# Optimization experiments

Hardware: AMD Instinct MI355X
Metric: run time of the kernel (lower is better)

The kernel has to match this reference:

```python
import jax, jax.numpy as jnp
import numpy as np

N_ITERATIONS = 3  # matches init_kwargs n_iterations


def squash(s):
    # s: [batch, output_caps, output_dim]
    sq = jnp.sum(s * s, axis=2, keepdims=True)          # [b, oc, 1]
    return s * (sq / (1.0 + sq) / jnp.sqrt(sq))


def setup_inputs() -> dict:
    key = jax.random.key(0)
    k_u, = jax.random.split(key, 1)
    batch, ic, oc, od = 128, 2048, 32, 16
    u_predict = jax.random.normal(k_u, (batch, ic, oc, od), dtype=jnp.float32)
    b = jnp.zeros((ic, oc), dtype=jnp.float32)  # routing logit prior, init zeros per torch module
    return {"u_predict": u_predict, "b": b}


def reference(u_predict, b):
    # u_predict: [batch, input_caps, output_caps, output_dim]; b: [input_caps, output_caps]
    batch = u_predict.shape[0]
    c = jax.nn.softmax(b, axis=1)                              # softmax over output_caps (torch implicit dim=1 on 2D)
    s = jnp.einsum('io,biod->bod', c, u_predict)               # weighted sum over input_caps
    v = squash(s)
    b_batch = jnp.broadcast_to(b, (batch,) + b.shape)          # [b, ic, oc]
    for _ in range(N_ITERATIONS):
        b_batch = b_batch + jnp.einsum('biod,bod->bio', u_predict, v)  # agreement
        c = jax.nn.softmax(b_batch, axis=-1)                   # coupling coeffs over output_caps
        s = jnp.einsum('bio,biod->bod', c, u_predict)
        v = squash(s)
    return v
```

## Files before the change

kernel.cpp:

```cpp
#include <hip/hip_runtime.h>
#include <math.h>


namespace {
constexpr int BATCH = 128;
constexpr int IC    = 2048;
constexpr int OC    = 32;
constexpr int OD    = 16;
constexpr int ROW   = OC * OD;
constexpr int BPB   = 16;
constexpr int ROWS_PER_BLOCK = IC / BPB;
constexpr int NWAVES = 4;

typedef _Float16 half8 __attribute__((ext_vector_type(8)));
typedef float    f32x4 __attribute__((ext_vector_type(4)));

constexpr size_t OFF_U16  = 0;
constexpr size_t OFF_PART = 268435456;
constexpr size_t OFF_W    = OFF_PART + 4194304;
constexpr size_t OFF_C0   = OFF_W + 262144;
}

__global__ void __launch_bounds__(256)
softmax_b(const float* __restrict__ blogit, float* __restrict__ c0)
{
    const int idx = blockIdx.x * 256 + threadIdx.x;
    float x = blogit[idx];
    float m = x;
#pragma unroll
    for (int off = 1; off <= 16; off <<= 1)
        m = fmaxf(m, __shfl_xor(m, off, 64));
    float e = __expf(x - m);
    float s = e;
#pragma unroll
    for (int off = 1; off <= 16; off <<= 1)
        s += __shfl_xor(s, off, 64);
    c0[idx] = e / s;
}

__global__ void __launch_bounds__(256)
pass0_convert(const float* __restrict__ u, const float* __restrict__ c0,
              _Float16* __restrict__ u16, float* __restrict__ partials)
{
    const int tid = threadIdx.x, lane = tid & 63, wave = tid >> 6;
    const int b = blockIdx.x >> 4, chunk = blockIdx.x & 15;
    const int o = lane >> 1, elem0 = lane * 8;
    const int i_base = chunk * ROWS_PER_BLOCK + wave * 32;

    f32x4 acc0 = {0.f,0.f,0.f,0.f}, acc1 = {0.f,0.f,0.f,0.f};

    const float*  ubase = u   + ((size_t)b * IC + i_base) * ROW + elem0;
    _Float16*     obase = u16 + ((size_t)b * IC + i_base) * ROW + elem0;

#pragma unroll 4
    for (int r = 0; r < 32; ++r) {
        const float* up = ubase + (size_t)r * ROW;
        f32x4 u0 = __builtin_nontemporal_load((const f32x4*)up);
        f32x4 u1 = __builtin_nontemporal_load((const f32x4*)(up + 4));
        float c = c0[(i_base + r) * OC + o];
        acc0 += c * u0;
        acc1 += c * u1;
        half8 h;
        h[0]=(_Float16)u0[0]; h[1]=(_Float16)u0[1]; h[2]=(_Float16)u0[2]; h[3]=(_Float16)u0[3];
        h[4]=(_Float16)u1[0]; h[5]=(_Float16)u1[1]; h[6]=(_Float16)u1[2]; h[7]=(_Float16)u1[3];
        __builtin_nontemporal_store(h, (half8*)(obase + (size_t)r * ROW));
    }

    __shared__ float red[NWAVES * ROW];
    float* my = red + wave * ROW + elem0;
    *(f32x4*)my       = acc0;
    *(f32x4*)(my + 4) = acc1;
    __syncthreads();
    float* dst = partials + (size_t)blockIdx.x * ROW;
    for (int p = tid; p < ROW; p += 256)
        dst[p] = red[p] + red[ROW + p] + red[2*ROW + p] + red[3*ROW + p];
}

__global__ void __launch_bounds__(256)
pass_iter(const _Float16* __restrict__ u16, const float* __restrict__ blogit,
          const float* __restrict__ w, float* __restrict__ partials)
{
    const int tid = threadIdx.x, lane = tid & 63, wave = tid >> 6;
    const int b = blockIdx.x >> 4, chunk = blockIdx.x & 15;
    const int o = lane >> 1, elem0 = lane * 8;
    const int i_base = chunk * ROWS_PER_BLOCK + wave * 32;

    const float* wp = w + (size_t)b * ROW + elem0;
    const f32x4 w0 = *(const f32x4*)wp;
    const f32x4 w1 = *(const f32x4*)(wp + 4);

    f32x4 acc0 = {0.f,0.f,0.f,0.f}, acc1 = {0.f,0.f,0.f,0.f};

    const half8* ubase = (const half8*)(u16 + ((size_t)b * IC + i_base) * ROW + elem0);

    half8 cur[4];
    cur[0] = ubase[0*64]; cur[1] = ubase[1*64]; cur[2] = ubase[2*64]; cur[3] = ubase[3*64];

    for (int g = 0; g < 8; ++g) {
        half8 nxt[4];
        if (g < 7) {
            const half8* p = ubase + (size_t)(g + 1) * 4 * 64;
            nxt[0] = p[0*64]; nxt[1] = p[1*64]; nxt[2] = p[2*64]; nxt[3] = p[3*64];
        }
        float blg[4];
#pragma unroll
        for (int r = 0; r < 4; ++r)
            blg[r] = blogit[(i_base + g*4 + r) * OC + o];

#pragma unroll
        for (int r = 0; r < 4; ++r) {
            float uf[8];
#pragma unroll
            for (int j = 0; j < 8; ++j) uf[j] = (float)cur[r][j];
            float part = uf[0]*w0[0] + uf[1]*w0[1] + uf[2]*w0[2] + uf[3]*w0[3]
                       + uf[4]*w1[0] + uf[5]*w1[1] + uf[6]*w1[2] + uf[7]*w1[3];
            float bb = blg[r] + part + __shfl_xor(part, 1, 64);
            float e = __expf(bb);
            float ssum = e;
#pragma unroll
            for (int off = 2; off <= 32; off <<= 1)
                ssum += __shfl_xor(ssum, off, 64);
            const float c = e / ssum;
            acc0[0] += c*uf[0]; acc0[1] += c*uf[1]; acc0[2] += c*uf[2]; acc0[3] += c*uf[3];
            acc1[0] += c*uf[4]; acc1[1] += c*uf[5]; acc1[2] += c*uf[6]; acc1[3] += c*uf[7];
        }
#pragma unroll
        for (int r = 0; r < 4; ++r) cur[r] = nxt[r];
    }

    __shared__ float red[NWAVES * ROW];
    float* my = red + wave * ROW + elem0;
    *(f32x4*)my       = acc0;
    *(f32x4*)(my + 4) = acc1;
    __syncthreads();
    float* dst = partials + (size_t)blockIdx.x * ROW;
    for (int p = tid; p < ROW; p += 256)
        dst[p] = red[p] + red[ROW + p] + red[2*ROW + p] + red[3*ROW + p];
}

template<int MODE>
__global__ void __launch_bounds__(256)
reduce_squash(const float* __restrict__ partials, float* __restrict__ w,
              float* __restrict__ out)
{
    const int idx = blockIdx.x * 256 + threadIdx.x;
    const int b = idx >> 9, p = idx & 511;
    const float* pp = partials + (size_t)(b * BPB) * ROW + p;
    float s = 0.f;
#pragma unroll
    for (int k = 0; k < BPB; ++k) s += pp[k * ROW];
    float sq = s * s;
    sq += __shfl_xor(sq, 1, 64);
    sq += __shfl_xor(sq, 2, 64);
    sq += __shfl_xor(sq, 4, 64);
    sq += __shfl_xor(sq, 8, 64);
    const float v = s * (sqrtf(sq) / (1.0f + sq));
    if (MODE == 0)      w[idx] = v;
    else if (MODE == 1) w[idx] += v;
    else                out[idx] = v;
}

extern "C" void kernel_launch(void* const* d_in, const int* in_sizes, int n_in,
                              void* d_out, int out_size, void* d_ws, size_t ws_size,
                              hipStream_t stream)
{
    const float* u  = (const float*)d_in[0];
    const float* bl = (const float*)d_in[1];
    float* out = (float*)d_out;

    char* ws = (char*)d_ws;
    _Float16* u16     = (_Float16*)(ws + OFF_U16);
    float*    partials= (float*)(ws + OFF_PART);
    float*    wbuf    = (float*)(ws + OFF_W);
    float*    c0      = (float*)(ws + OFF_C0);

    const dim3 blk(256);
    const dim3 gpass(BATCH * BPB);
    const dim3 gred(BATCH * ROW / 256);

    softmax_b   <<<dim3(IC * OC / 256), blk, 0, stream>>>(bl, c0);
    pass0_convert<<<gpass, blk, 0, stream>>>(u, c0, u16, partials);
    reduce_squash<0><<<gred, blk, 0, stream>>>(partials, wbuf, out);
    pass_iter   <<<gpass, blk, 0, stream>>>(u16, bl, wbuf, partials);
    reduce_squash<1><<<gred, blk, 0, stream>>>(partials, wbuf, out);
    pass_iter   <<<gpass, blk, 0, stream>>>(u16, bl, wbuf, partials);
    reduce_squash<1><<<gred, blk, 0, stream>>>(partials, wbuf, out);
    pass_iter   <<<gpass, blk, 0, stream>>>(u16, bl, wbuf, partials);
    reduce_squash<2><<<gred, blk, 0, stream>>>(partials, wbuf, out);
}
```

Measured before the change: 858.2 us.

## Fuse reduce/squash into iteration kernels and inline initial softmax

```diff
diff --git a/kernel.cpp b/kernel.cpp
--- a/kernel.cpp
+++ b/kernel.cpp
@@ -6,40 +6,25 @@
 constexpr int BATCH = 128;
 constexpr int IC    = 2048;
 constexpr int OC    = 32;
-constexpr int OD    = 16;
-constexpr int ROW   = OC * OD;
+constexpr int ROW   = 512;
 constexpr int BPB   = 16;
 constexpr int ROWS_PER_BLOCK = IC / BPB;
 constexpr int NWAVES = 4;
+constexpr int HROW  = ROW / 8;
 
 typedef _Float16 half8 __attribute__((ext_vector_type(8)));
 typedef float    f32x4 __attribute__((ext_vector_type(4)));
 
-constexpr size_t OFF_U16  = 0;
-constexpr size_t OFF_PART = 268435456;
-constexpr size_t OFF_W    = OFF_PART + 4194304;
-constexpr size_t OFF_C0   = OFF_W + 262144;
+constexpr size_t OFF_U16    = 0;
+constexpr size_t PART_BYTES = (size_t)BATCH * BPB * ROW * 4;
+constexpr size_t OFF_P0     = 268435456;
+constexpr size_t OFF_P1     = OFF_P0 + PART_BYTES;
+constexpr size_t OFF_WA     = OFF_P1 + PART_BYTES;
+constexpr size_t OFF_WB     = OFF_WA + 262144;
 }
 
 __global__ void __launch_bounds__(256)
-softmax_b(const float* __restrict__ blogit, float* __restrict__ c0)
-{
-    const int idx = blockIdx.x * 256 + threadIdx.x;
-    float x = blogit[idx];
-    float m = x;
-#pragma unroll
-    for (int off = 1; off <= 16; off <<= 1)
-        m = fmaxf(m, __shfl_xor(m, off, 64));
-    float e = __expf(x - m);
-    float s = e;
-#pragma unroll
-    for (int off = 1; off <= 16; off <<= 1)
-        s += __shfl_xor(s, off, 64);
-    c0[idx] = e / s;
-}
-
-__global__ void __launch_bounds__(256)
-pass0_convert(const float* __restrict__ u, const float* __restrict__ c0,
+pass0_convert(const float* __restrict__ u, const float* __restrict__ blogit,
               _Float16* __restrict__ u16, float* __restrict__ partials)
 {
     const int tid = threadIdx.x, lane = tid & 63, wave = tid >> 6;
@@ -57,7 +42,12 @@
         const float* up = ubase + (size_t)r * ROW;
         f32x4 u0 = __builtin_nontemporal_load((const f32x4*)up);
         f32x4 u1 = __builtin_nontemporal_load((const f32x4*)(up + 4));
-        float c = c0[(i_base + r) * OC + o];
+        float e = __expf(blogit[(i_base + r) * OC + o]);
+        float ssum = e;
+#pragma unroll
+        for (int off = 2; off <= 32; off <<= 1)
+            ssum += __shfl_xor(ssum, off, 64);
+        const float c = e / ssum;
         acc0 += c * u0;
         acc1 += c * u1;
         half8 h;
@@ -76,31 +66,73 @@
         dst[p] = red[p] + red[ROW + p] + red[2*ROW + p] + red[3*ROW + p];
 }
 
+template<int IT>
+__device__ __forceinline__ void compute_w(const float* __restrict__ part_in,
+                                          const float* __restrict__ w_in,
+                                          float* __restrict__ w_out,
+                                          float* __restrict__ wlds,
+                                          int b, int tid, int chunk)
+{
+    const int p = tid * 2;
+    const float* pp = part_in + (size_t)b * (BPB * ROW) + p;
+    float s0 = 0.f, s1 = 0.f;
+#pragma unroll
+    for (int k = 0; k < BPB; ++k) {
+        s0 += pp[(size_t)k * ROW];
+        s1 += pp[(size_t)k * ROW + 1];
+    }
+    float sq = s0 * s0 + s1 * s1;
+    sq += __shfl_xor(sq, 1, 64);
+    sq += __shfl_xor(sq, 2, 64);
+    sq += __shfl_xor(sq, 4, 64);
+    const float sc = sqrtf(sq) / (1.0f + sq);
+    float w0 = s0 * sc, w1 = s1 * sc;
+    if (IT > 1) {
+        w0 += w_in[b * ROW + p];
+        w1 += w_in[b * ROW + p + 1];
+    }
+    wlds[p]     = w0;
+    wlds[p + 1] = w1;
+    if (IT < 3 && chunk == 0) {
+        w_out[b * ROW + p]     = w0;
+        w_out[b * ROW + p + 1] = w1;
+    }
+}
+
+template<int IT>
 __global__ void __launch_bounds__(256)
 pass_iter(const _Float16* __restrict__ u16, const float* __restrict__ blogit,
-          const float* __restrict__ w, float* __restrict__ partials)
+          const float* __restrict__ part_in, const float* __restrict__ w_in,
+          float* __restrict__ part_out, float* __restrict__ w_out)
 {
     const int tid = threadIdx.x, lane = tid & 63, wave = tid >> 6;
     const int b = blockIdx.x >> 4, chunk = blockIdx.x & 15;
     const int o = lane >> 1, elem0 = lane * 8;
     const int i_base = chunk * ROWS_PER_BLOCK + wave * 32;
 
-    const float* wp = w + (size_t)b * ROW + elem0;
-    const f32x4 w0 = *(const f32x4*)wp;
-    const f32x4 w1 = *(const f32x4*)(wp + 4);
+    __shared__ float red[NWAVES * ROW];
+    __shared__ float wlds[ROW];
+
+    const half8* ubase = (const half8*)(u16 + ((size_t)b * IC + i_base) * ROW + elem0);
+
+    half8 cur[4];
+    cur[0] = ubase[0*HROW]; cur[1] = ubase[1*HROW];
+    cur[2] = ubase[2*HROW]; cur[3] = ubase[3*HROW];
+
+    compute_w<IT>(part_in, w_in, w_out, wlds, b, tid, chunk);
+    __syncthreads();
+
+    const f32x4 w0 = *(const f32x4*)(wlds + elem0);
+    const f32x4 w1 = *(const f32x4*)(wlds + elem0 + 4);
 
     f32x4 acc0 = {0.f,0.f,0.f,0.f}, acc1 = {0.f,0.f,0.f,0.f};
-
-    const half8* ubase = (const half8*)(u16 + ((size_t)b * IC + i_base) * ROW + elem0);
-
-    half8 cur[4];
-    cur[0] = ubase[0*64]; cur[1] = ubase[1*64]; cur[2] = ubase[2*64]; cur[3] = ubase[3*64];
 
     for (int g = 0; g < 8; ++g) {
         half8 nxt[4];
         if (g < 7) {
-            const half8* p = ubase + (size_t)(g + 1) * 4 * 64;
-            nxt[0] = p[0*64]; nxt[1] = p[1*64]; nxt[2] = p[2*64]; nxt[3] = p[3*64];
+            const half8* ptr = ubase + (size_t)(g + 1) * 4 * HROW;
+            nxt[0] = ptr[0*HROW]; nxt[1] = ptr[1*HROW];
+            nxt[2] = ptr[2*HROW]; nxt[3] = ptr[3*HROW];
         }
         float blg[4];
 #pragma unroll
@@ -128,36 +160,30 @@
         for (int r = 0; r < 4; ++r) cur[r] = nxt[r];
     }
 
-    __shared__ float red[NWAVES * ROW];
     float* my = red + wave * ROW + elem0;
     *(f32x4*)my       = acc0;
     *(f32x4*)(my + 4) = acc1;
     __syncthreads();
-    float* dst = partials + (size_t)blockIdx.x * ROW;
+    float* dst = part_out + (size_t)blockIdx.x * ROW;
     for (int p = tid; p < ROW; p += 256)
         dst[p] = red[p] + red[ROW + p] + red[2*ROW + p] + red[3*ROW + p];
 }
 
-template<int MODE>
 __global__ void __launch_bounds__(256)
-reduce_squash(const float* __restrict__ partials, float* __restrict__ w,
-              float* __restrict__ out)
+reduce_out(const float* __restrict__ partials, float* __restrict__ out)
 {
     const int idx = blockIdx.x * 256 + threadIdx.x;
     const int b = idx >> 9, p = idx & 511;
     const float* pp = partials + (size_t)(b * BPB) * ROW + p;
     float s = 0.f;
 #pragma unroll
-    for (int k = 0; k < BPB; ++k) s += pp[k * ROW];
+    for (int k = 0; k < BPB; ++k) s += pp[(size_t)k * ROW];
     float sq = s * s;
     sq += __shfl_xor(sq, 1, 64);
     sq += __shfl_xor(sq, 2, 64);
     sq += __shfl_xor(sq, 4, 64);
     sq += __shfl_xor(sq, 8, 64);
-    const float v = s * (sqrtf(sq) / (1.0f + sq));
-    if (MODE == 0)      w[idx] = v;
-    else if (MODE == 1) w[idx] += v;
-    else                out[idx] = v;
+    out[idx] = s * (sqrtf(sq) / (1.0f + sq));
 }
 
 extern "C" void kernel_launch(void* const* d_in, const int* in_sizes, int n_in,
@@ -169,22 +195,18 @@
     float* out = (float*)d_out;
 
     char* ws = (char*)d_ws;
-    _Float16* u16     = (_Float16*)(ws + OFF_U16);
-    float*    partials= (float*)(ws + OFF_PART);
-    float*    wbuf    = (float*)(ws + OFF_W);
-    float*    c0      = (float*)(ws + OFF_C0);
+    _Float16* u16 = (_Float16*)(ws + OFF_U16);
+    float* part0  = (float*)(ws + OFF_P0);
+    float* part1  = (float*)(ws + OFF_P1);
+    float* wA     = (float*)(ws + OFF_WA);
+    float* wB     = (float*)(ws + OFF_WB);
 
     const dim3 blk(256);
     const dim3 gpass(BATCH * BPB);
-    const dim3 gred(BATCH * ROW / 256);
-
-    softmax_b   <<<dim3(IC * OC / 256), blk, 0, stream>>>(bl, c0);
-    pass0_convert<<<gpass, blk, 0, stream>>>(u, c0, u16, partials);
-    reduce_squash<0><<<gred, blk, 0, stream>>>(partials, wbuf, out);
-    pass_iter   <<<gpass, blk, 0, stream>>>(u16, bl, wbuf, partials);
-    reduce_squash<1><<<gred, blk, 0, stream>>>(partials, wbuf, out);
-    pass_iter   <<<gpass, blk, 0, stream>>>(u16, bl, wbuf, partials);
-    reduce_squash<1><<<gred, blk, 0, stream>>>(partials, wbuf, out);
-    pass_iter   <<<gpass, blk, 0, stream>>>(u16, bl, wbuf, partials);
-    reduce_squash<2><<<gred, blk, 0, stream>>>(partials, wbuf, out);
-}
+
+    pass0_convert<<<gpass, blk, 0, stream>>>(u, bl, u16, part0);
+    pass_iter<1> <<<gpass, blk, 0, stream>>>(u16, bl, part0, nullptr, part1, wA);
+    pass_iter<2> <<<gpass, blk, 0, stream>>>(u16, bl, part1, wA,      part0, wB);
+    pass_iter<3> <<<gpass, blk, 0, stream>>>(u16, bl, part0, wB,      part1, nullptr);
+    reduce_out   <<<dim3(BATCH * ROW / 256), blk, 0, stream>>>(part1, out);
+}
```

After: 871.0 us. Within noise of the previous version (+1.5%).
